# Performance work log

Measured on AMD Instinct MI355X. Metric: run time of the kernel, lower is better.

## Reference

```python
import jax, jax.numpy as jnp
import numpy as np

B, T, D = 2, 2048, 1024
N_HEADS, N_KV_HEADS = 16, 4
D_HEAD = D // N_HEADS            # 64
N_GROUPS = N_HEADS // N_KV_HEADS  # 4
ROPE_THETA = 10000.0


def _rope_freqs(t, d_head, theta):
    inv = 1.0 / (theta ** (jnp.arange(0, d_head, 2, dtype=jnp.float32) / d_head))  # (d_head/2,)
    ang = jnp.arange(t, dtype=jnp.float32)[:, None] * inv[None, :]                 # (T, d_head/2)
    return jnp.stack([jnp.cos(ang), jnp.sin(ang)], axis=-1)                        # (T, d_head/2, 2)


def _apply_rope(x, freqs):
    # x: (B, T, H, d_head); freqs: (T, d_head/2, 2) = (cos, sin)
    xr = x.reshape(*x.shape[:-1], -1, 2)          # (B,T,H,d/2,2)
    xre, xim = xr[..., 0], xr[..., 1]
    fre = freqs[None, :, None, :, 0]              # (1,T,1,d/2)
    fim = freqs[None, :, None, :, 1]
    outre = xre * fre - xim * fim
    outim = xre * fim + xim * fre
    return jnp.stack([outre, outim], axis=-1).reshape(x.shape)


def setup_inputs() -> dict:
    key = jax.random.key(0)
    ks = jax.random.split(key, 5)
    x = jax.random.normal(ks[0], (B, T, D), dtype=jnp.float32)
    w_q = jax.random.normal(ks[1], (N_HEADS * D_HEAD, D), dtype=jnp.float32) * 0.02
    w_k = jax.random.normal(ks[2], (N_KV_HEADS * D_HEAD, D), dtype=jnp.float32) * 0.02
    w_v = jax.random.normal(ks[3], (N_KV_HEADS * D_HEAD, D), dtype=jnp.float32) * 0.02
    w_o = jax.random.normal(ks[4], (D, N_HEADS * D_HEAD), dtype=jnp.float32) * 0.02
    rope_freqs = _rope_freqs(T, D_HEAD, ROPE_THETA)
    causal = jnp.tril(jnp.ones((T, T), dtype=bool))
    mask = jnp.where(causal, 0.0, -1e9).astype(jnp.float32)[None, None]  # (1,1,T,T)
    return {"x": x, "rope_freqs": rope_freqs, "mask": mask,
            "w_q": w_q, "w_k": w_k, "w_v": w_v, "w_o": w_o}


def reference(x, rope_freqs, mask, w_q, w_k, w_v, w_o):
    # projections (torch Linear: y = x @ W.T)
    q = jnp.einsum('btd,od->bto', x, w_q).reshape(B, T, N_HEADS, D_HEAD)
    k = jnp.einsum('btd,od->bto', x, w_k).reshape(B, T, N_KV_HEADS, D_HEAD)
    v = jnp.einsum('btd,od->bto', x, w_v).reshape(B, T, N_KV_HEADS, D_HEAD)
    q = _apply_rope(q, rope_freqs)
    k = _apply_rope(k, rope_freqs)
    # GQA: expand KV heads (kv head h -> N_GROUPS contiguous query heads)
    k = jnp.repeat(k, N_GROUPS, axis=2)   # (B,T,H,d)
    v = jnp.repeat(v, N_GROUPS, axis=2)
    q = q.transpose(0, 2, 1, 3)           # (B,H,T,d)
    k = k.transpose(0, 2, 1, 3)
    v = v.transpose(0, 2, 1, 3)
    scale = 1.0 / np.sqrt(D_HEAD).astype(np.float32)
    scores = jnp.einsum('bhqd,bhkd->bhqk', q, k) * scale + mask
    attn = jax.nn.softmax(scores, axis=-1)
    out = jnp.einsum('bhqk,bhkd->bhqd', attn, v)
    out = out.transpose(0, 2, 1, 3).reshape(B, T, N_HEADS * D_HEAD)
    return jnp.einsum('bto,do->btd', out, w_o)
```

## Files before the change

### kernel.cpp

```cpp
#include <hip/hip_runtime.h>
#include <hip/hip_bf16.h>
#include <cstddef>
#include <type_traits>

#define TT   2048
#define NH   16
#define NKV  4
#define DH   64

typedef __bf16 bf16x8 __attribute__((ext_vector_type(8)));
typedef float  f32x4  __attribute__((ext_vector_type(4)));

#if __has_builtin(__builtin_amdgcn_exp2f)
#define EXP2F(x) __builtin_amdgcn_exp2f(x)
#else
#define EXP2F(x) __expf((x) * 0.69314718056f)
#endif

#define QSCALE 0.180336880f

__global__ __launch_bounds__(256)
void cast_kernel(const float* __restrict__ x,  const float* __restrict__ wq,
                 const float* __restrict__ wk, const float* __restrict__ wv,
                 const float* __restrict__ wo,
                 __bf16* __restrict__ xb, __bf16* __restrict__ wqkv,
                 __bf16* __restrict__ wob)
{
    const int g = blockIdx.x * 256 + threadIdx.x;
    const float* src;
    __bf16* dst;
    int off;
    if (g < 1048576)       { src = x;  dst = xb;   off = g; }
    else if (g < 1310720)  { src = wq; dst = wqkv; off = g - 1048576; }
    else if (g < 1376256)  { src = wk; dst = wqkv + 1048576; off = g - 1310720; }
    else if (g < 1441792)  { src = wv; dst = wqkv + 1310720; off = g - 1376256; }
    else                   { src = wo; dst = wob;  off = g - 1441792; }
    const float4 v = *(const float4*)(src + (size_t)off * 4);
    union { __bf16 h[4]; uint2 u; } o;
    o.h[0] = (__bf16)v.x; o.h[1] = (__bf16)v.y;
    o.h[2] = (__bf16)v.z; o.h[3] = (__bf16)v.w;
    *(uint2*)(dst + (size_t)off * 4) = o.u;
}

template<int MODE>
__global__ __launch_bounds__(128, 2)
void mm_kernel(const __bf16* __restrict__ A,
               const __bf16* __restrict__ W,
               const float* __restrict__ rope,
               void* __restrict__ O0, void* __restrict__ O1,
               void* __restrict__ O2)
{
    constexpr int K  = 1024;
    constexpr int NK = K / 32;
    __shared__ __bf16 As[2][64 * 32];
    __shared__ __bf16 Bs[2][128 * 32];

    const int tid  = threadIdx.x;
    const int lane = tid & 63;
    const int wv   = tid >> 6;
    const int quad = lane >> 4;
    const int lc   = lane & 15;
    const int gm0  = blockIdx.y * 64;
    const int gn0  = blockIdx.x * 128;
    const int wc0  = wv * 64;

    size_t gaA[2], gaB[4];
    int lsA[2], lsB[4];
#pragma unroll
    for (int j = 0; j < 2; j++) {
        const int p = tid + j * 128;
        const int r = p >> 2, q = (p & 3) ^ ((r >> 1) & 3);
        gaA[j] = (size_t)r * K + q * 8;
        lsA[j] = p * 8;
    }
#pragma unroll
    for (int j = 0; j < 4; j++) {
        const int p = tid + j * 128;
        const int r = p >> 2, q = (p & 3) ^ ((r >> 1) & 3);
        gaB[j] = (size_t)r * K + q * 8;
        lsB[j] = p * 8;
    }
    const __bf16* Ag = A + (size_t)gm0 * K;
    const __bf16* Wg = W + (size_t)gn0 * K;

    auto foff = [&](int row) { return (row * 4 + (quad ^ ((row >> 1) & 3))) * 8; };
    int aoff[4], boff[4];
#pragma unroll
    for (int i = 0; i < 4; i++) {
        aoff[i] = foff(i * 16 + lc);
        boff[i] = foff(wc0 + i * 16 + lc);
    }

    f32x4 acc[4][4];
#pragma unroll
    for (int i = 0; i < 4; i++)
#pragma unroll
        for (int j = 0; j < 4; j++) acc[i][j] = (f32x4){0.f, 0.f, 0.f, 0.f};

    bf16x8 ar[2][2], br[2][4];

#pragma unroll
    for (int j = 0; j < 2; j++) ar[0][j] = *(const bf16x8*)(Ag + gaA[j]);
#pragma unroll
    for (int j = 0; j < 4; j++) br[0][j] = *(const bf16x8*)(Wg + gaB[j]);
#pragma unroll
    for (int j = 0; j < 2; j++) *(bf16x8*)&As[0][lsA[j]] = ar[0][j];
#pragma unroll
    for (int j = 0; j < 4; j++) *(bf16x8*)&Bs[0][lsB[j]] = br[0][j];
#pragma unroll
    for (int j = 0; j < 2; j++) ar[1][j] = *(const bf16x8*)(Ag + gaA[j] + 32);
#pragma unroll
    for (int j = 0; j < 4; j++) br[1][j] = *(const bf16x8*)(Wg + gaB[j] + 32);
#pragma unroll
    for (int j = 0; j < 2; j++) ar[0][j] = *(const bf16x8*)(Ag + gaA[j] + 64);
#pragma unroll
    for (int j = 0; j < 4; j++) br[0][j] = *(const bf16x8*)(Wg + gaB[j] + 64);
    __syncthreads();

    auto step = [&](int kt, auto pc) {
        constexpr int P = decltype(pc)::value;
        constexpr int Q = 1 - P;
        bf16x8 af[4], bfr[4];
#pragma unroll
        for (int i = 0; i < 4; i++) af[i]  = *(const bf16x8*)&As[P][aoff[i]];
#pragma unroll
        for (int j = 0; j < 4; j++) bfr[j] = *(const bf16x8*)&Bs[P][boff[j]];
        if (kt + 1 < NK) {
#pragma unroll
            for (int j = 0; j < 2; j++) *(bf16x8*)&As[Q][lsA[j]] = ar[Q][j];
#pragma unroll
            for (int j = 0; j < 4; j++) *(bf16x8*)&Bs[Q][lsB[j]] = br[Q][j];
        }
#pragma unroll
        for (int i = 0; i < 4; i++)
#pragma unroll
            for (int j = 0; j < 4; j++)
                acc[i][j] = __builtin_amdgcn_mfma_f32_16x16x32_bf16(
                    af[i], bfr[j], acc[i][j], 0, 0, 0);
        if (kt + 3 < NK) {
            const int kb = (kt + 3) * 32;
#pragma unroll
            for (int j = 0; j < 2; j++) ar[Q][j] = *(const bf16x8*)(Ag + gaA[j] + kb);
#pragma unroll
            for (int j = 0; j < 4; j++) br[Q][j] = *(const bf16x8*)(Wg + gaB[j] + kb);
        }
        if (kt + 1 < NK) __syncthreads();
    };
    for (int kt = 0; kt < NK; kt += 2) {
        step(kt,     std::integral_constant<int, 0>{});
        step(kt + 1, std::integral_constant<int, 1>{});
    }

    if (MODE == 0) {
        __bf16* Qo = (__bf16*)O0;
        __bf16* Ko = (__bf16*)O1;
        __bf16* Vo = (__bf16*)O2;
        const int region = (gn0 < 1024) ? 0 : (gn0 < 1280) ? 1 : 2;
#pragma unroll
        for (int i = 0; i < 4; i++) {
#pragma unroll
            for (int r = 0; r < 4; r++) {
                const int grow = gm0 + i * 16 + quad * 4 + r;
                const int b = grow >> 11, t = grow & 2047;
                const float* rrow = rope + t * 64;
#pragma unroll
                for (int j = 0; j < 4; j++) {
                    const float v = acc[i][j][r];
                    const float partner = __shfl_xor(v, 1, 64);
                    const int col = gn0 + wc0 + j * 16 + lc;
                    if (region == 0) {
                        const int h = col >> 6, d = col & 63;
                        const float2 cs = *(const float2*)(rrow + (d >> 1) * 2);
                        const float out = v * cs.x + partner * ((d & 1) ? cs.y : -cs.y);
                        Qo[((size_t)(b * NH + h) * TT + t) * DH + d] = (__bf16)(out * QSCALE);
                    } else if (region == 1) {
                        const int ck = col - 1024;
                        const int kh = ck >> 6, d = ck & 63;
                        const float2 cs = *(const float2*)(rrow + (d >> 1) * 2);
                        const float out = v * cs.x + partner * ((d & 1) ? cs.y : -cs.y);
                        Ko[((size_t)(b * NKV + kh) * TT + t) * DH + d] = (__bf16)out;
                    } else {
                        const int cv = col - 1280;
                        const int kh = cv >> 6, d = cv & 63;
                        Vo[((size_t)(b * NKV + kh) * DH + d) * TT + t] = (__bf16)v;
                    }
                }
            }
        }
    } else {
        float* Of = (float*)O0;
#pragma unroll
        for (int i = 0; i < 4; i++)
#pragma unroll
            for (int r = 0; r < 4; r++) {
                const int grow = gm0 + i * 16 + quad * 4 + r;
#pragma unroll
                for (int j = 0; j < 4; j++)
                    Of[(size_t)grow * 1024 + gn0 + wc0 + j * 16 + lc] = acc[i][j][r];
            }
    }
}

__global__ __launch_bounds__(128, 2)
void attn_kernel(const __bf16* __restrict__ Q,
                 const __bf16* __restrict__ K,
                 const __bf16* __restrict__ Vt,
                 __bf16* __restrict__ O)
{
    __shared__ __bf16 Ks[64 * 64];
    __shared__ __bf16 Vs[64 * 64];
    __shared__ __bf16 Ps[2][32][72];

    const int tid  = threadIdx.x;
    const int lane = tid & 63;
    const int wv   = tid >> 6;
    const int quad = lane >> 4;
    const int lc   = lane & 15;

    const int a   = blockIdx.x & 31;
    const int rep = blockIdx.x >> 5;
    const int qt  = ((rep >> 3) & 1) ? (31 - a) : a;
    const int b   = rep >> 4;
    const int h   = rep & 15;
    const int kh  = h >> 2;
    const int nk  = qt + 1;

    const __bf16* Kg = K  + (size_t)(b * NKV + kh) * TT * DH;
    const __bf16* Vg = Vt + (size_t)(b * NKV + kh) * DH * TT;

    bf16x8 qb[2][2];
#pragma unroll
    for (int u = 0; u < 2; u++) {
        const __bf16* qp = Q + ((size_t)(b * NH + h) * TT
                                + qt * 64 + wv * 32 + u * 16 + lc) * DH;
        qb[u][0] = *(const bf16x8*)(qp + quad * 8);
        qb[u][1] = *(const bf16x8*)(qp + 32 + quad * 8);
    }

    int koff[4], voff[4], lsl[4];
#pragma unroll
    for (int j = 0; j < 4; j++) {
        const int p  = tid + j * 128;
        const int r  = p >> 3;
        const int qs = (p & 7) ^ (r & 7);
        koff[j] = r * DH + qs * 8;
        voff[j] = r * TT + qs * 8;
        lsl[j]  = p * 8;
    }

    int foff[4][2];
#pragma unroll
    for (int g = 0; g < 4; g++)
#pragma unroll
        for (int c = 0; c < 2; c++)
            foff[g][c] = ((g * 16 + lc) * 8 + ((c * 4 + quad) ^ (lc & 7))) * 8;

    float l_s[2] = {0.f, 0.f};
    f32x4 oacc[2][4];
#pragma unroll
    for (int u = 0; u < 2; u++)
#pragma unroll
        for (int g = 0; g < 4; g++) oacc[u][g] = (f32x4){0.f, 0.f, 0.f, 0.f};

    bf16x8 kr[4], vr[4];
    auto load_regs = [&](int kt) {
        const __bf16* kp = Kg + (size_t)kt * 64 * DH;
        const __bf16* vp = Vg + (size_t)kt * 64;
#pragma unroll
        for (int j = 0; j < 4; j++) {
            kr[j] = *(const bf16x8*)(kp + koff[j]);
            vr[j] = *(const bf16x8*)(vp + voff[j]);
        }
    };
    auto store_lds = [&]() {
#pragma unroll
        for (int j = 0; j < 4; j++) {
            *(bf16x8*)&Ks[lsl[j]] = kr[j];
            *(bf16x8*)&Vs[lsl[j]] = vr[j];
        }
    };

    load_regs(0);
    store_lds();
    if (nk > 1) load_regs(1);
    __syncthreads();

    for (int kt = 0; kt < nk; kt++) {
        bf16x8 ka[4][2];
#pragma unroll
        for (int g = 0; g < 4; g++) {
            ka[g][0] = *(const bf16x8*)&Ks[foff[g][0]];
            ka[g][1] = *(const bf16x8*)&Ks[foff[g][1]];
        }

        const int Dbase = qt * 64 + wv * 32 - kt * 64;

        f32x4 s[2][4];
#pragma unroll
        for (int u = 0; u < 2; u++)
#pragma unroll
            for (int g = 0; g < 4; g++) {
                f32x4 z = (f32x4){0.f, 0.f, 0.f, 0.f};
                z = __builtin_amdgcn_mfma_f32_16x16x32_bf16(ka[g][0], qb[u][0], z, 0, 0, 0);
                z = __builtin_amdgcn_mfma_f32_16x16x32_bf16(ka[g][1], qb[u][1], z, 0, 0, 0);
                s[u][g] = z;
            }

#pragma unroll
        for (int u = 0; u < 2; u++) {
            const int D = Dbase + u * 16;
            if (D < 63) {
                const int thr = D + lc;
#pragma unroll
                for (int g = 0; g < 4; g++)
#pragma unroll
                    for (int r = 0; r < 4; r++)
                        if (g * 16 + quad * 4 + r > thr) s[u][g][r] = -1e30f;
            }
        }

#pragma unroll
        for (int u = 0; u < 2; u++) {
            float rs = 0.f;
#pragma unroll
            for (int g = 0; g < 4; g++) {
#pragma unroll
                for (int r = 0; r < 4; r++) {
                    s[u][g][r] = EXP2F(s[u][g][r]);
                    rs += s[u][g][r];
                }
                union { __bf16 hh[4]; uint2 uu; } pk;
                pk.hh[0] = (__bf16)s[u][g][0]; pk.hh[1] = (__bf16)s[u][g][1];
                pk.hh[2] = (__bf16)s[u][g][2]; pk.hh[3] = (__bf16)s[u][g][3];
                *(uint2*)&Ps[wv][u * 16 + lc][g * 16 + quad * 4] = pk.uu;
            }
            l_s[u] += rs;
        }

        bf16x8 va[4][2];
#pragma unroll
        for (int g = 0; g < 4; g++) {
            va[g][0] = *(const bf16x8*)&Vs[foff[g][0]];
            va[g][1] = *(const bf16x8*)&Vs[foff[g][1]];
        }

#pragma unroll
        for (int u = 0; u < 2; u++) {
            const bf16x8 pb0 = *(const bf16x8*)&Ps[wv][u * 16 + lc][quad * 8];
            const bf16x8 pb1 = *(const bf16x8*)&Ps[wv][u * 16 + lc][32 + quad * 8];
#pragma unroll
            for (int g = 0; g < 4; g++) {
                oacc[u][g] = __builtin_amdgcn_mfma_f32_16x16x32_bf16(va[g][0], pb0, oacc[u][g], 0, 0, 0);
                oacc[u][g] = __builtin_amdgcn_mfma_f32_16x16x32_bf16(va[g][1], pb1, oacc[u][g], 0, 0, 0);
            }
        }

        if (kt + 1 < nk) {
            __syncthreads();
            store_lds();
            if (kt + 2 < nk) load_regs(kt + 2);
            __syncthreads();
        }
    }

#pragma unroll
    for (int u = 0; u < 2; u++) {
        float l = l_s[u];
        l += __shfl_xor(l, 16, 64);
        l += __shfl_xor(l, 32, 64);
        const float inv = 1.f / l;
        const int t = qt * 64 + wv * 32 + u * 16 + lc;
        __bf16* op = O + (size_t)(b * TT + t) * (NH * DH) + h * DH;
#pragma unroll
        for (int g = 0; g < 4; g++) {
            union { __bf16 hh[4]; uint2 uu; } pk;
            pk.hh[0] = (__bf16)(oacc[u][g][0] * inv);
            pk.hh[1] = (__bf16)(oacc[u][g][1] * inv);
            pk.hh[2] = (__bf16)(oacc[u][g][2] * inv);
            pk.hh[3] = (__bf16)(oacc[u][g][3] * inv);
            *(uint2*)(op + g * 16 + quad * 4) = pk.uu;
        }
    }
}

extern "C" void kernel_launch(void* const* d_in, const int* in_sizes, int n_in,
                              void* d_out, int out_size, void* d_ws, size_t ws_size,
                              hipStream_t stream)
{
    const float* x    = (const float*)d_in[0];
    const float* rope = (const float*)d_in[1];
    const float* w_q  = (const float*)d_in[3];
    const float* w_k  = (const float*)d_in[4];
    const float* w_v  = (const float*)d_in[5];
    const float* w_o  = (const float*)d_in[6];
    float* out = (float*)d_out;

    char* ws = (char*)d_ws;
    __bf16* Qb   = (__bf16*)(ws);
    __bf16* Kb   = (__bf16*)(ws + (8  << 20));
    __bf16* Vtb  = (__bf16*)(ws + (10 << 20));
    __bf16* AOb  = (__bf16*)(ws + (12 << 20));
    __bf16* xb   = (__bf16*)(ws + (20 << 20));
    __bf16* Wqkv = (__bf16*)(ws + (28 << 20));
    __bf16* Wob  = (__bf16*)(ws + (31 << 20));

    cast_kernel<<<6656, dim3(256), 0, stream>>>(x, w_q, w_k, w_v, w_o,
                                                xb, Wqkv, Wob);

    dim3 g1(12, 64);
    mm_kernel<0><<<g1, dim3(128), 0, stream>>>(xb, Wqkv, rope,
                                               (void*)Qb, (void*)Kb, (void*)Vtb);

    attn_kernel<<<1024, dim3(128), 0, stream>>>(Qb, Kb, Vtb, AOb);

    dim3 g3(8, 64);
    mm_kernel<1><<<g3, dim3(128), 0, stream>>>(AOb, Wob, rope,
                                               (void*)out, nullptr, nullptr);
}
```

Baseline: 185.7 us.

## Use four waves per GEMM tile and remap blocks for XCD-aware scheduling

The projection GEMM kernel now runs with 256 threads (four waves) per 64x128 tile instead of two. Each wave computes a 64x32 slice, which halves the accumulator and fragment registers per thread and raises the occupancy hint. It also permutes the linear block index so consecutive blocks are spread across the eight XCDs in groups, aiming for better L2 reuse of A and W tiles. In exchange, each wave does less MFMA work per LDS fragment load, so A fragments are re-read by more waves.

```diff
diff --git a/kernel.cpp b/kernel.cpp
--- a/kernel.cpp
+++ b/kernel.cpp
@@ -43,7 +43,7 @@
 }
 
 template<int MODE>
-__global__ __launch_bounds__(128, 2)
+__global__ __launch_bounds__(256, 3)
 void mm_kernel(const __bf16* __restrict__ A,
                const __bf16* __restrict__ W,
                const float* __restrict__ rope,
@@ -52,6 +52,7 @@
 {
     constexpr int K  = 1024;
     constexpr int NK = K / 32;
+    constexpr int NX = (MODE == 0) ? 12 : 8;
     __shared__ __bf16 As[2][64 * 32];
     __shared__ __bf16 Bs[2][128 * 32];
 
@@ -60,22 +61,27 @@
     const int wv   = tid >> 6;
     const int quad = lane >> 4;
     const int lc   = lane & 15;
-    const int gm0  = blockIdx.y * 64;
-    const int gn0  = blockIdx.x * 128;
-    const int wc0  = wv * 64;
-
-    size_t gaA[2], gaB[4];
-    int lsA[2], lsB[4];
+
+    const int dlin = blockIdx.x + NX * blockIdx.y;
+    const int nid  = (dlin & 7) * ((NX * 64) >> 3) + (dlin >> 3);
+    const int bx   = nid % NX;
+    const int by   = nid / NX;
+
+    const int gm0  = by * 64;
+    const int gn0  = bx * 128;
+    const int wc0  = wv * 32;
+
+    size_t gaA;  int lsA;
+    {
+        const int p = tid;
+        const int r = p >> 2, q = (p & 3) ^ ((r >> 1) & 3);
+        gaA = (size_t)r * K + q * 8;
+        lsA = p * 8;
+    }
+    size_t gaB[2]; int lsB[2];
 #pragma unroll
     for (int j = 0; j < 2; j++) {
-        const int p = tid + j * 128;
-        const int r = p >> 2, q = (p & 3) ^ ((r >> 1) & 3);
-        gaA[j] = (size_t)r * K + q * 8;
-        lsA[j] = p * 8;
-    }
-#pragma unroll
-    for (int j = 0; j < 4; j++) {
-        const int p = tid + j * 128;
+        const int p = tid + j * 256;
         const int r = p >> 2, q = (p & 3) ^ ((r >> 1) & 3);
         gaB[j] = (size_t)r * K + q * 8;
         lsB[j] = p * 8;
@@ -84,65 +90,58 @@
     const __bf16* Wg = W + (size_t)gn0 * K;
 
     auto foff = [&](int row) { return (row * 4 + (quad ^ ((row >> 1) & 3))) * 8; };
-    int aoff[4], boff[4];
-#pragma unroll
-    for (int i = 0; i < 4; i++) {
-        aoff[i] = foff(i * 16 + lc);
-        boff[i] = foff(wc0 + i * 16 + lc);
-    }
-
-    f32x4 acc[4][4];
+    int aoff[4], boff[2];
+#pragma unroll
+    for (int i = 0; i < 4; i++) aoff[i] = foff(i * 16 + lc);
+#pragma unroll
+    for (int j = 0; j < 2; j++) boff[j] = foff(wc0 + j * 16 + lc);
+
+    f32x4 acc[4][2];
 #pragma unroll
     for (int i = 0; i < 4; i++)
 #pragma unroll
-        for (int j = 0; j < 4; j++) acc[i][j] = (f32x4){0.f, 0.f, 0.f, 0.f};
-
-    bf16x8 ar[2][2], br[2][4];
-
-#pragma unroll
-    for (int j = 0; j < 2; j++) ar[0][j] = *(const bf16x8*)(Ag + gaA[j]);
-#pragma unroll
-    for (int j = 0; j < 4; j++) br[0][j] = *(const bf16x8*)(Wg + gaB[j]);
-#pragma unroll
-    for (int j = 0; j < 2; j++) *(bf16x8*)&As[0][lsA[j]] = ar[0][j];
-#pragma unroll
-    for (int j = 0; j < 4; j++) *(bf16x8*)&Bs[0][lsB[j]] = br[0][j];
-#pragma unroll
-    for (int j = 0; j < 2; j++) ar[1][j] = *(const bf16x8*)(Ag + gaA[j] + 32);
-#pragma unroll
-    for (int j = 0; j < 4; j++) br[1][j] = *(const bf16x8*)(Wg + gaB[j] + 32);
-#pragma unroll
-    for (int j = 0; j < 2; j++) ar[0][j] = *(const bf16x8*)(Ag + gaA[j] + 64);
-#pragma unroll
-    for (int j = 0; j < 4; j++) br[0][j] = *(const bf16x8*)(Wg + gaB[j] + 64);
+        for (int j = 0; j < 2; j++) acc[i][j] = (f32x4){0.f, 0.f, 0.f, 0.f};
+
+    bf16x8 ar[2], br[2][2];
+
+    ar[0] = *(const bf16x8*)(Ag + gaA);
+#pragma unroll
+    for (int j = 0; j < 2; j++) br[0][j] = *(const bf16x8*)(Wg + gaB[j]);
+    *(bf16x8*)&As[0][lsA] = ar[0];
+#pragma unroll
+    for (int j = 0; j < 2; j++) *(bf16x8*)&Bs[0][lsB[j]] = br[0][j];
+    ar[1] = *(const bf16x8*)(Ag + gaA + 32);
+#pragma unroll
+    for (int j = 0; j < 2; j++) br[1][j] = *(const bf16x8*)(Wg + gaB[j] + 32);
+    ar[0] = *(const bf16x8*)(Ag + gaA + 64);
+#pragma unroll
+    for (int j = 0; j < 2; j++) br[0][j] = *(const bf16x8*)(Wg + gaB[j] + 64);
     __syncthreads();
 
     auto step = [&](int kt, auto pc) {
         constexpr int P = decltype(pc)::value;
         constexpr int Q = 1 - P;
-        bf16x8 af[4], bfr[4];
+        bf16x8 af[4], bfr[2];
 #pragma unroll
         for (int i = 0; i < 4; i++) af[i]  = *(const bf16x8*)&As[P][aoff[i]];
 #pragma unroll
-        for (int j = 0; j < 4; j++) bfr[j] = *(const bf16x8*)&Bs[P][boff[j]];
+        for (int j = 0; j < 2; j++) bfr[j] = *(const bf16x8*)&Bs[P][boff[j]];
         if (kt + 1 < NK) {
-#pragma unroll
-            for (int j = 0; j < 2; j++) *(bf16x8*)&As[Q][lsA[j]] = ar[Q][j];
-#pragma unroll
-            for (int j = 0; j < 4; j++) *(bf16x8*)&Bs[Q][lsB[j]] = br[Q][j];
+            *(bf16x8*)&As[Q][lsA] = ar[Q];
+#pragma unroll
+            for (int j = 0; j < 2; j++) *(bf16x8*)&Bs[Q][lsB[j]] = br[Q][j];
         }
 #pragma unroll
         for (int i = 0; i < 4; i++)
 #pragma unroll
-            for (int j = 0; j < 4; j++)
+            for (int j = 0; j < 2; j++)
                 acc[i][j] = __builtin_amdgcn_mfma_f32_16x16x32_bf16(
                     af[i], bfr[j], acc[i][j], 0, 0, 0);
         if (kt + 3 < NK) {
             const int kb = (kt + 3) * 32;
-#pragma unroll
-            for (int j = 0; j < 2; j++) ar[Q][j] = *(const bf16x8*)(Ag + gaA[j] + kb);
-#pragma unroll
-            for (int j = 0; j < 4; j++) br[Q][j] = *(const bf16x8*)(Wg + gaB[j] + kb);
+            ar[Q] = *(const bf16x8*)(Ag + gaA + kb);
+#pragma unroll
+            for (int j = 0; j < 2; j++) br[Q][j] = *(const bf16x8*)(Wg + gaB[j] + kb);
         }
         if (kt + 1 < NK) __syncthreads();
     };
@@ -164,7 +163,7 @@
                 const int b = grow >> 11, t = grow & 2047;
                 const float* rrow = rope + t * 64;
 #pragma unroll
-                for (int j = 0; j < 4; j++) {
+                for (int j = 0; j < 2; j++) {
                     const float v = acc[i][j][r];
                     const float partner = __shfl_xor(v, 1, 64);
                     const int col = gn0 + wc0 + j * 16 + lc;
@@ -195,7 +194,7 @@
             for (int r = 0; r < 4; r++) {
                 const int grow = gm0 + i * 16 + quad * 4 + r;
 #pragma unroll
-                for (int j = 0; j < 4; j++)
+                for (int j = 0; j < 2; j++)
                     Of[(size_t)grow * 1024 + gn0 + wc0 + j * 16 + lc] = acc[i][j][r];
             }
     }
@@ -408,12 +407,12 @@
                                                 xb, Wqkv, Wob);
 
     dim3 g1(12, 64);
-    mm_kernel<0><<<g1, dim3(128), 0, stream>>>(xb, Wqkv, rope,
+    mm_kernel<0><<<g1, dim3(256), 0, stream>>>(xb, Wqkv, rope,
                                                (void*)Qb, (void*)Kb, (void*)Vtb);
 
     attn_kernel<<<1024, dim3(128), 0, stream>>>(Qb, Kb, Vtb, AOb);
 
     dim3 g3(8, 64);
-    mm_kernel<1><<<g3, dim3(128), 0, stream>>>(AOb, Wob, rope,
+    mm_kernel<1><<<g3, dim3(256), 0, stream>>>(AOb, Wob, rope,
                                                (void*)out, nullptr, nullptr);
 }
```

Result: faster. 173.1 us (-6.8%).
